# Kernel optimization log

Measured on AMD Instinct MI355X. Metric: run time of the kernel, lower is better.

## Reference

```python
import jax, jax.numpy as jnp
import numpy as np

B, C_IN, C_OUT, H, W, K = 64, 64, 128, 64, 64, 3


def setup_inputs() -> dict:
    key = jax.random.key(0)
    k1, k2, k3 = jax.random.split(key, 3)
    x = jax.random.normal(k1, (B, C_IN, H, W), dtype=jnp.float32)
    weight = jax.random.normal(k2, (C_OUT, C_IN, K, K), dtype=jnp.float32)
    bias = jax.random.normal(k3, (C_OUT, 1, 1), dtype=jnp.float32)
    return {"x": x, "weight": weight, "bias": bias}


def reference(x, weight, bias):
    # Valid (no pad), stride-1, NCHW direct conv + broadcast bias, matching
    # the naive nested-loop conv2d_multi_in_out + bias of MyConv2D.
    out = jax.lax.conv_general_dilated(
        x, weight,
        window_strides=(1, 1),
        padding="VALID",
        dimension_numbers=("NCHW", "OIHW", "NCHW"),
    )
    return out + bias  # bias (C_out,1,1) broadcasts over (B, C_out, H_out, W_out)
```

## Files before the change

### kernel.cpp

```cpp
#include <hip/hip_runtime.h>

#define CI 64
#define CO 128
#define HH 64
#define WW 64
#define OH 62
#define OW 62
#define XTW 66
#define RB (XTW * 64)
#define ROWS_OUT 4
#define ROWS_IN 6
#define NBLK_X 16

typedef __attribute__((ext_vector_type(8))) short short8x;
typedef __attribute__((ext_vector_type(16))) float f32x16;

__device__ __attribute__((aligned(16))) ushort g_wt[9 * CO * CI];
__device__ __attribute__((aligned(16))) ushort g_xt[64 * 64 * XTW * 64];

__device__ __forceinline__ ushort bf16rne(float f) {
    unsigned u = __builtin_bit_cast(unsigned, f);
    u += 0x7fffu + ((u >> 16) & 1u);
    return (ushort)(u >> 16);
}

__device__ __forceinline__ void gld_lds16(const ushort* g, ushort* l) {
    __builtin_amdgcn_global_load_lds(
        (const __attribute__((address_space(1))) unsigned*)g,
        (__attribute__((address_space(3))) unsigned*)l, 16, 0, 0);
}

__global__ __launch_bounds__(256)
void wprep(const float* __restrict__ w) {
    const int idx = blockIdx.x * 256 + threadIdx.x;
    const int kk = idx >> 13;
    const int rem = idx & 8191;
    const int co = rem >> 6, ci = rem & 63;
    g_wt[idx] = bf16rne(w[(co * 64 + ci) * 9 + kk]);
}

__global__ __launch_bounds__(256)
void xprep(const float* __restrict__ x) {
    __shared__ ushort T[64 * 68];
    const int t = threadIdx.x;
    const int h = blockIdx.x, b = blockIdx.y;
    const float* xb = x + ((size_t)b * 64 * 64 + h) * 64;

    #pragma unroll
    for (int g = 0; g < 4; ++g) {
        const int ci = g * 16 + (t >> 4);
        const int w0 = (t & 15) * 4;
        const float4 v = *(const float4*)(xb + (size_t)ci * 4096 + w0);
        ushort tmp[4];
        tmp[0] = bf16rne(v.x); tmp[1] = bf16rne(v.y);
        tmp[2] = bf16rne(v.z); tmp[3] = bf16rne(v.w);
        *reinterpret_cast<uint2*>(&T[ci * 68 + w0]) = *reinterpret_cast<const uint2*>(tmp);
    }
    __syncthreads();

    ushort* dst = g_xt + (size_t)(b * 64 + h) * XTW * 64;
    #pragma unroll
    for (int g = 0; g < 2; ++g) {
        const int w = g * 32 + (t >> 3);
        const int cg = t & 7;
        ushort tmp[8];
        #pragma unroll
        for (int j = 0; j < 8; ++j) tmp[j] = T[(cg * 8 + j) * 68 + w];
        *reinterpret_cast<uint4*>(dst + w * 64 + cg * 8) = *reinterpret_cast<const uint4*>(tmp);
    }
    if (t < 16) {
        const uint4 z{0, 0, 0, 0};
        *reinterpret_cast<uint4*>(dst + 64 * 64 + t * 8) = z;
    }
}

__global__ __launch_bounds__(256, 2)
void conv_fused(const float* __restrict__ bias, float* __restrict__ out) {
    __shared__ ushort Xl[ROWS_IN * RB];
    __shared__ float  sB[CO];

    const int tid = threadIdx.x;
    const int wv = tid >> 6, L = tid & 63, l31 = L & 31, q = L >> 5;
    const int h = wv >> 1;
    const int rw = wv & 1;
    const int b = blockIdx.y, oh0 = blockIdx.x * ROWS_OUT;

    if (tid < CO) sB[tid] = bias[tid];

    const ushort* wbase = g_wt + (h * 64 + l31) * 64 + q * 8;
    short8x wbuf[2][8];
    #pragma unroll
    for (int m = 0; m < 2; ++m)
        #pragma unroll
        for (int ss = 0; ss < 4; ++ss)
            wbuf[0][m * 4 + ss] = *(const short8x*)(wbase + m * 2048 + ss * 16);

    const ushort* xb = g_xt + (size_t)(b * 64) * RB;
    #pragma unroll
    for (int j = 0; j < 12; ++j) {
        const int i = j * 256 + tid;
        const int pl = i >> 3, c = i & 7;
        const int r6 = pl / 66;
        const int px = pl - r6 * 66;
        int ir = oh0 + r6;
        if (ir > 63) ir = 63;
        gld_lds16(xb + (size_t)ir * RB + px * 64 + ((c ^ (pl & 7)) * 8),
                  &Xl[(size_t)(j * 256 + (tid & 192)) * 8]);
    }
    if (tid < 96) {
        const int i = 3072 + tid;
        const int pl = i >> 3, c = i & 7;
        const int r6 = pl / 66;
        const int px = pl - r6 * 66;
        int ir = oh0 + r6;
        if (ir > 63) ir = 63;
        gld_lds16(xb + (size_t)ir * RB + px * 64 + ((c ^ (pl & 7)) * 8),
                  &Xl[(size_t)(3072 + (tid & 192)) * 8]);
    }

    f32x16 acc[2][2][2];
    #pragma unroll
    for (int r2 = 0; r2 < 2; ++r2)
        #pragma unroll
        for (int i = 0; i < 2; ++i)
            #pragma unroll
            for (int jj = 0; jj < 2; ++jj)
                #pragma unroll
                for (int r = 0; r < 16; ++r) acc[r2][i][jj][r] = 0.f;

    __syncthreads();

    #pragma unroll
    for (int kk = 0; kk < 9; ++kk) {
        const short8x* wf = wbuf[kk & 1];
        if (kk < 8) {
            const ushort* nb = wbase + (kk + 1) * (CO * CI);
            #pragma unroll
            for (int m = 0; m < 2; ++m)
                #pragma unroll
                for (int ss = 0; ss < 4; ++ss)
                    wbuf[(kk + 1) & 1][m * 4 + ss] = *(const short8x*)(nb + m * 2048 + ss * 16);
        }
        const int kr = kk / 3, kc = kk - kr * 3;
        const int pBa = (rw + kr) * XTW + kc + l31;
        const int pBb = (rw + 2 + kr) * XTW + kc + l31;
        const ushort* bPa = Xl + pBa * 64;
        const ushort* bPb = Xl + pBb * 64;
        const int f0a = pBa & 7, f0b = pBb & 7;
        #pragma unroll
        for (int ss = 0; ss < 4; ++ss) {
            const int oba = (((ss * 2 + q) ^ f0a) * 8);
            const int obb = (((ss * 2 + q) ^ f0b) * 8);
            short8x a0 = *(const short8x*)(bPa + oba);
            short8x a1 = *(const short8x*)(bPa + 32 * 64 + oba);
            short8x c0 = *(const short8x*)(bPb + obb);
            short8x c1 = *(const short8x*)(bPb + 32 * 64 + obb);
            acc[0][0][0] = __builtin_amdgcn_mfma_f32_32x32x16_bf16(wf[ss],     a0, acc[0][0][0], 0, 0, 0);
            acc[0][0][1] = __builtin_amdgcn_mfma_f32_32x32x16_bf16(wf[ss],     a1, acc[0][0][1], 0, 0, 0);
            acc[0][1][0] = __builtin_amdgcn_mfma_f32_32x32x16_bf16(wf[4 + ss], a0, acc[0][1][0], 0, 0, 0);
            acc[0][1][1] = __builtin_amdgcn_mfma_f32_32x32x16_bf16(wf[4 + ss], a1, acc[0][1][1], 0, 0, 0);
            acc[1][0][0] = __builtin_amdgcn_mfma_f32_32x32x16_bf16(wf[ss],     c0, acc[1][0][0], 0, 0, 0);
            acc[1][0][1] = __builtin_amdgcn_mfma_f32_32x32x16_bf16(wf[ss],     c1, acc[1][0][1], 0, 0, 0);
            acc[1][1][0] = __builtin_amdgcn_mfma_f32_32x32x16_bf16(wf[4 + ss], c0, acc[1][1][0], 0, 0, 0);
            acc[1][1][1] = __builtin_amdgcn_mfma_f32_32x32x16_bf16(wf[4 + ss], c1, acc[1][1][1], 0, 0, 0);
        }
    }

    #pragma unroll
    for (int r2 = 0; r2 < 2; ++r2) {
        const int oh = oh0 + rw + 2 * r2;
        if (oh < OH) {
            #pragma unroll
            for (int mt = 0; mt < 2; ++mt)
                #pragma unroll
                for (int nt = 0; nt < 2; ++nt) {
                    const int col = nt * 32 + l31;
                    if (col < OW) {
                        #pragma unroll
                        for (int reg = 0; reg < 16; ++reg) {
                            const int co = h * 64 + mt * 32 + 4 * q + (reg & 3) + 8 * (reg >> 2);
                            out[(((size_t)b * CO + co) * OH + oh) * OW + col] = acc[r2][mt][nt][reg] + sB[co];
                        }
                    }
                }
        }
    }
}

extern "C" void kernel_launch(void* const* d_in, const int* in_sizes, int n_in,
                              void* d_out, int out_size, void* d_ws, size_t ws_size,
                              hipStream_t stream) {
    const float* x    = (const float*)d_in[0];
    const float* wgt  = (const float*)d_in[1];
    const float* bias = (const float*)d_in[2];
    float* out = (float*)d_out;

    wprep<<<dim3(288), 256, 0, stream>>>(wgt);
    xprep<<<dim3(64, 64), 256, 0, stream>>>(x);
    conv_fused<<<dim3(NBLK_X, 64), 256, 0, stream>>>(bias, out);
}
```

Baseline: 258.1 us.

## Fuse input bf16 conversion and transpose into conv kernel, drop xprep pass

```diff
diff --git a/kernel.cpp b/kernel.cpp
--- a/kernel.cpp
+++ b/kernel.cpp
@@ -16,18 +16,11 @@
 typedef __attribute__((ext_vector_type(16))) float f32x16;
 
 __device__ __attribute__((aligned(16))) ushort g_wt[9 * CO * CI];
-__device__ __attribute__((aligned(16))) ushort g_xt[64 * 64 * XTW * 64];
 
 __device__ __forceinline__ ushort bf16rne(float f) {
     unsigned u = __builtin_bit_cast(unsigned, f);
     u += 0x7fffu + ((u >> 16) & 1u);
     return (ushort)(u >> 16);
-}
-
-__device__ __forceinline__ void gld_lds16(const ushort* g, ushort* l) {
-    __builtin_amdgcn_global_load_lds(
-        (const __attribute__((address_space(1))) unsigned*)g,
-        (__attribute__((address_space(3))) unsigned*)l, 16, 0, 0);
 }
 
 __global__ __launch_bounds__(256)
@@ -39,43 +32,9 @@
     g_wt[idx] = bf16rne(w[(co * 64 + ci) * 9 + kk]);
 }
 
-__global__ __launch_bounds__(256)
-void xprep(const float* __restrict__ x) {
-    __shared__ ushort T[64 * 68];
-    const int t = threadIdx.x;
-    const int h = blockIdx.x, b = blockIdx.y;
-    const float* xb = x + ((size_t)b * 64 * 64 + h) * 64;
-
-    #pragma unroll
-    for (int g = 0; g < 4; ++g) {
-        const int ci = g * 16 + (t >> 4);
-        const int w0 = (t & 15) * 4;
-        const float4 v = *(const float4*)(xb + (size_t)ci * 4096 + w0);
-        ushort tmp[4];
-        tmp[0] = bf16rne(v.x); tmp[1] = bf16rne(v.y);
-        tmp[2] = bf16rne(v.z); tmp[3] = bf16rne(v.w);
-        *reinterpret_cast<uint2*>(&T[ci * 68 + w0]) = *reinterpret_cast<const uint2*>(tmp);
-    }
-    __syncthreads();
-
-    ushort* dst = g_xt + (size_t)(b * 64 + h) * XTW * 64;
-    #pragma unroll
-    for (int g = 0; g < 2; ++g) {
-        const int w = g * 32 + (t >> 3);
-        const int cg = t & 7;
-        ushort tmp[8];
-        #pragma unroll
-        for (int j = 0; j < 8; ++j) tmp[j] = T[(cg * 8 + j) * 68 + w];
-        *reinterpret_cast<uint4*>(dst + w * 64 + cg * 8) = *reinterpret_cast<const uint4*>(tmp);
-    }
-    if (t < 16) {
-        const uint4 z{0, 0, 0, 0};
-        *reinterpret_cast<uint4*>(dst + 64 * 64 + t * 8) = z;
-    }
-}
-
 __global__ __launch_bounds__(256, 2)
-void conv_fused(const float* __restrict__ bias, float* __restrict__ out) {
+void conv_fused(const float* __restrict__ x, const float* __restrict__ bias,
+                float* __restrict__ out) {
     __shared__ ushort Xl[ROWS_IN * RB];
     __shared__ float  sB[CO];
 
@@ -95,27 +54,33 @@
         for (int ss = 0; ss < 4; ++ss)
             wbuf[0][m * 4 + ss] = *(const short8x*)(wbase + m * 2048 + ss * 16);
 
-    const ushort* xb = g_xt + (size_t)(b * 64) * RB;
-    #pragma unroll
-    for (int j = 0; j < 12; ++j) {
-        const int i = j * 256 + tid;
-        const int pl = i >> 3, c = i & 7;
-        const int r6 = pl / 66;
-        const int px = pl - r6 * 66;
-        int ir = oh0 + r6;
-        if (ir > 63) ir = 63;
-        gld_lds16(xb + (size_t)ir * RB + px * 64 + ((c ^ (pl & 7)) * 8),
-                  &Xl[(size_t)(j * 256 + (tid & 192)) * 8]);
+    if (tid < 96) {
+        const int r6 = tid >> 4, c = tid & 15;
+        const int px = 64 + (c >> 3), slot = c & 7;
+        const uint4 z{0, 0, 0, 0};
+        *reinterpret_cast<uint4*>(&Xl[(r6 * XTW + px) * 64 + slot * 8]) = z;
     }
-    if (tid < 96) {
-        const int i = 3072 + tid;
-        const int pl = i >> 3, c = i & 7;
-        const int r6 = pl / 66;
-        const int px = pl - r6 * 66;
-        int ir = oh0 + r6;
-        if (ir > 63) ir = 63;
-        gld_lds16(xb + (size_t)ir * RB + px * 64 + ((c ^ (pl & 7)) * 8),
-                  &Xl[(size_t)(3072 + (tid & 192)) * 8]);
+
+    {
+        const int w = L;
+        const size_t cibase = (size_t)(b * 64 + wv * 16) * (HH * WW);
+        #pragma unroll
+        for (int r6 = 0; r6 < ROWS_IN; ++r6) {
+            int ir = oh0 + r6;
+            if (ir > 63) ir = 63;
+            const float* src = x + cibase + (size_t)ir * WW + w;
+            union { ushort u[8]; uint4 v; } p0, p1;
+            #pragma unroll
+            for (int k = 0; k < 8; ++k)
+                p0.u[k] = bf16rne(src[(size_t)k * (HH * WW)]);
+            #pragma unroll
+            for (int k = 0; k < 8; ++k)
+                p1.u[k] = bf16rne(src[(size_t)(8 + k) * (HH * WW)]);
+            const int pl = r6 * XTW + w, key = pl & 7;
+            ushort* dst = &Xl[pl * 64];
+            *reinterpret_cast<uint4*>(dst + (((2 * wv)     ^ key) * 8)) = p0.v;
+            *reinterpret_cast<uint4*>(dst + (((2 * wv + 1) ^ key) * 8)) = p1.v;
+        }
     }
 
     f32x16 acc[2][2][2];
@@ -196,6 +161,5 @@
     float* out = (float*)d_out;
 
     wprep<<<dim3(288), 256, 0, stream>>>(wgt);
-    xprep<<<dim3(64, 64), 256, 0, stream>>>(x);
-    conv_fused<<<dim3(NBLK_X, 64), 256, 0, stream>>>(bias, out);
+    conv_fused<<<dim3(NBLK_X, 64), 256, 0, stream>>>(x, bias, out);
 }
```

Result: faster. 217.2 us (-15.8%).
